# Optimization experiments

Hardware: AMD Instinct MI355X
Metric: run time of the kernel (lower is better)

Reference implementation:

```python
import jax, jax.numpy as jnp
import numpy as np

N, D, P, R, T, K = 200000, 128, 4096, 4, 3, 16

def setup_inputs() -> dict:
    key = jax.random.key(0)
    ks = jax.random.split(key, 9)
    return {
        "node_embeds": jax.random.normal(ks[0], (N, D), jnp.float32),
        "node_pairs": jax.random.randint(ks[1], (P, 2), 0, N),
        "node_type_ids": jax.random.randint(ks[2], (N,), 0, T),
        "neighbor_idx": jax.random.randint(ks[3], (P, 2, R, K), 0, N),
        "delta_t": jax.random.uniform(ks[4], (P, 2, R, K), jnp.float32),
        "W_phi": jax.random.normal(ks[5], (T, D, D), jnp.float32) * 0.05,
        "W_zeta": jax.random.normal(ks[6], (2 * D,), jnp.float32) * 0.05,
        "W_beta_w": jax.random.normal(ks[7], (R, D, D), jnp.float32) * 0.05,
        "W_beta_b": jax.random.normal(ks[8], (R, D), jnp.float32) * 0.05,
    }

def reference(node_embeds, node_pairs, node_type_ids, neighbor_idx, delta_t,
              W_phi, W_zeta, W_beta_w, W_beta_b):
    n = node_embeds.shape[0]
    # per-node type-specific linear: compute all types then select (T small)
    H_all = jnp.einsum('nd,tde->tne', node_embeds, W_phi)        # [T,N,D]
    H = H_all[node_type_ids, jnp.arange(n)]                      # [N,D]
    # micro attention: e = W_zeta([h_n; h_s]) * exp(-dt), softmax over K neighbors
    zn, zs = W_zeta[:D], W_zeta[D:]
    h_n = H[neighbor_idx]                                        # [P,2,R,K,D]
    e_n = jnp.einsum('psrkd,d->psrk', h_n, zn)
    e_s = jnp.einsum('psd,d->ps', H[node_pairs], zs)             # [P,2]
    e = (e_n + e_s[:, :, None, None]) * jnp.exp(-delta_t)        # [P,2,R,K]
    alpha = jax.nn.softmax(e, axis=-1)
    # meso: attention-weighted aggregation per relation, then per-relation linear
    h_nei = node_embeds[neighbor_idx]                            # [P,2,R,K,D]
    h_agg = jnp.einsum('psrk,psrkd->psrd', alpha, h_nei)         # [P,2,R,D]
    h_beta = jnp.einsum('psrd,rde->psre', h_agg, W_beta_w) + W_beta_b
    # macro: average over both pair sides and relations, sigmoid combine
    x_tilde = h_beta.mean(axis=(1, 2))                           # [P,D]
    return jax.nn.sigmoid(x_tilde)
```

## Files before the change

kernel.cpp:

```cpp
#include <hip/hip_runtime.h>
#include <hip/hip_bf16.h>

#define NN 200000
#define D 128
#define P 4096
#define R 4
#define T 3
#define K 16

__device__ __forceinline__ float bf2f(unsigned int u) {
    union { unsigned int i; float f; } c;
    c.i = u << 16;
    return c.f;
}
__device__ __forceinline__ unsigned short f2bf(float x) {
    union { float f; unsigned int i; } c; c.f = x;
    unsigned int r = c.i + 0x7FFFu + ((c.i >> 16) & 1u);
    return (unsigned short)(r >> 16);
}
__device__ __forceinline__ float ldE(const void* p, size_t i, int f32) {
    return f32 ? ((const float*)p)[i] : bf2f(((const unsigned short*)p)[i]);
}
__device__ __forceinline__ void ld8(const void* p, size_t off, int f32, float* o) {
    if (f32) {
        const float* q = (const float*)p + off;
        float4 a = *(const float4*)q;
        float4 b = *(const float4*)(q + 4);
        o[0]=a.x; o[1]=a.y; o[2]=a.z; o[3]=a.w;
        o[4]=b.x; o[5]=b.y; o[6]=b.z; o[7]=b.w;
    } else {
        uint4 r = *(const uint4*)((const unsigned short*)p + off);
        o[0]=bf2f(r.x & 0xffffu); o[1]=bf2f(r.x >> 16);
        o[2]=bf2f(r.y & 0xffffu); o[3]=bf2f(r.y >> 16);
        o[4]=bf2f(r.z & 0xffffu); o[5]=bf2f(r.z >> 16);
        o[6]=bf2f(r.w & 0xffffu); o[7]=bf2f(r.w >> 16);
    }
}

__global__ void prep_kernel(const unsigned short* __restrict__ emb_u,
                            const void* __restrict__ W_phi,
                            const void* __restrict__ W_zeta,
                            int* __restrict__ gflag,
                            float* __restrict__ ws_v, float* __restrict__ ws_u) {
    __shared__ int sbad[2];
    const int tid = threadIdx.x;
    const int t   = blockIdx.x;
    int bad = 0;
    #pragma unroll
    for (int i = 0; i < 4; ++i) {
        unsigned short u = emb_u[(size_t)(blockIdx.x * 512 + tid * 4 + i) * 2 * 97];
        unsigned int e = (u >> 7) & 0xFFu;
        if (e >= 147u) bad = 1;
    }
    int anyb = __any(bad) ? 1 : 0;
    if ((tid & 63) == 0) sbad[tid >> 6] = anyb;
    __syncthreads();
    const int f32 = sbad[0] | sbad[1];
    if (t == 0 && tid == 0) *gflag = f32;

    const int d = tid;
    const size_t rb = (size_t)(t * D + d) * D;
    float av = 0.f, au = 0.f;
    for (int e = 0; e < D; e += 8) {
        float w[8], zn[8], zs[8];
        ld8(W_phi, rb + e, f32, w);
        ld8(W_zeta, e, f32, zn);
        ld8(W_zeta, D + e, f32, zs);
        #pragma unroll
        for (int q = 0; q < 8; ++q) { av += w[q] * zn[q]; au += w[q] * zs[q]; }
    }
    ws_v[t * D + d] = av;
    ws_u[t * D + d] = au;
}

__global__ __launch_bounds__(512, 4) void fused_all(
    const void* __restrict__ emb,
    const int* __restrict__ pairs,
    const int* __restrict__ types,
    const int* __restrict__ nbr,
    const void* __restrict__ dlt,
    const void* __restrict__ W_bw,
    const void* __restrict__ W_bb,
    const float* __restrict__ ws_v,
    const float* __restrict__ ws_u,
    const int* __restrict__ flag,
    void* __restrict__ out)
{
    __shared__ __align__(16) float vsh[T * D];
    __shared__ __align__(16) float ush[T * D];
    __shared__ __align__(16) float gsh[2][R][D];
    __shared__ __align__(16) float gsum[R][D];
    __shared__ __align__(16) float ysh[R][D];

    const int f32  = *flag;
    const int tid  = threadIdx.x;
    const int wv   = tid >> 6;
    const int l    = tid & 63;
    const int s    = wv >> 2;
    const int r    = wv & 3;
    const int p    = blockIdx.x;
    const int rsub = l >> 4;
    const int ch   = l & 15;
    const int base = p * 2 * R * K + s * R * K + r * K;

    const int k   = l & 15;
    const int nb  = nbr[base + k];
    const float dtv = ldE(dlt, (size_t)(base + k), f32);
    const int ns  = pairs[p * 2 + s];

    int snb[4];
    #pragma unroll
    for (int i = 0; i < 4; ++i) snb[i] = __shfl(nb, i * 4 + rsub, 64);

    const unsigned short* eu = (const unsigned short*)emb;
    uint4 cur[4];
    if (!f32) {
        #pragma unroll
        for (int i = 0; i < 4; ++i)
            cur[i] = *(const uint4*)(eu + (size_t)snb[i] * D + ch * 8);
    }
    const int tp = types[nb];
    const int ts = types[ns];

    float ee0, ee1;
    if (!f32) {
        unsigned int w2 = *(const unsigned int*)(eu + (size_t)ns * D + 2 * l);
        ee0 = bf2f(w2 & 0xffffu); ee1 = bf2f(w2 >> 16);
    } else {
        float2 f2 = *(const float2*)((const float*)emb + (size_t)ns * D + 2 * l);
        ee0 = f2.x; ee1 = f2.y;
    }

    for (int i = tid; i < T * D; i += 512) { vsh[i] = ws_v[i]; ush[i] = ws_u[i]; }
    __syncthreads();

    float es;
    {
        float a = ee0 * ush[ts * D + 2 * l] + ee1 * ush[ts * D + 2 * l + 1];
        #pragma unroll
        for (int off = 1; off <= 32; off <<= 1) a += __shfl_xor(a, off, 64);
        es = a;
    }

    float sdt[4]; int stp[4];
    #pragma unroll
    for (int i = 0; i < 4; ++i) {
        sdt[i] = __shfl(dtv, i * 4 + rsub, 64);
        stp[i] = __shfl(tp,  i * 4 + rsub, 64);
    }

    float ef[4];
    if (!f32) {
        #pragma unroll
        for (int i = 0; i < 4; ++i) {
            const float* vp = vsh + stp[i] * D + ch * 8;
            float4 v0 = *(const float4*)vp;
            float4 v1 = *(const float4*)(vp + 4);
            float a = 0.f;
            a += bf2f(cur[i].x & 0xffffu) * v0.x + bf2f(cur[i].x >> 16) * v0.y;
            a += bf2f(cur[i].y & 0xffffu) * v0.z + bf2f(cur[i].y >> 16) * v0.w;
            a += bf2f(cur[i].z & 0xffffu) * v1.x + bf2f(cur[i].z >> 16) * v1.y;
            a += bf2f(cur[i].w & 0xffffu) * v1.z + bf2f(cur[i].w >> 16) * v1.w;
            #pragma unroll
            for (int off = 1; off <= 8; off <<= 1) a += __shfl_xor(a, off, 64);
            ef[i] = (a + es) * __expf(-sdt[i]);
        }
    } else {
        #pragma unroll
        for (int i = 0; i < 4; ++i) {
            const float* vp = vsh + stp[i] * D + ch * 8;
            float rv[8];
            ld8(emb, (size_t)snb[i] * D + ch * 8, 1, rv);
            float a = 0.f;
            #pragma unroll
            for (int q = 0; q < 8; ++q) a += rv[q] * vp[q];
            #pragma unroll
            for (int off = 1; off <= 8; off <<= 1) a += __shfl_xor(a, off, 64);
            ef[i] = (a + es) * __expf(-sdt[i]);
        }
    }

    float m = fmaxf(fmaxf(ef[0], ef[1]), fmaxf(ef[2], ef[3]));
    m = fmaxf(m, __shfl_xor(m, 16, 64));
    m = fmaxf(m, __shfl_xor(m, 32, 64));
    float al[4], ssum = 0.f;
    #pragma unroll
    for (int i = 0; i < 4; ++i) { al[i] = __expf(ef[i] - m); ssum += al[i]; }
    ssum += __shfl_xor(ssum, 16, 64);
    ssum += __shfl_xor(ssum, 32, 64);
    float inv = 1.f / ssum;

    float acc[8] = {0.f,0.f,0.f,0.f,0.f,0.f,0.f,0.f};
    if (!f32) {
        #pragma unroll
        for (int i = 0; i < 4; ++i) {
            float a = al[i] * inv;
            acc[0] += a * bf2f(cur[i].x & 0xffffu); acc[1] += a * bf2f(cur[i].x >> 16);
            acc[2] += a * bf2f(cur[i].y & 0xffffu); acc[3] += a * bf2f(cur[i].y >> 16);
            acc[4] += a * bf2f(cur[i].z & 0xffffu); acc[5] += a * bf2f(cur[i].z >> 16);
            acc[6] += a * bf2f(cur[i].w & 0xffffu); acc[7] += a * bf2f(cur[i].w >> 16);
        }
    } else {
        #pragma unroll
        for (int i = 0; i < 4; ++i) {
            float a = al[i] * inv;
            float rv[8];
            ld8(emb, (size_t)snb[i] * D + ch * 8, 1, rv);
            #pragma unroll
            for (int q = 0; q < 8; ++q) acc[q] += a * rv[q];
        }
    }
    #pragma unroll
    for (int q = 0; q < 8; ++q) {
        acc[q] += __shfl_xor(acc[q], 16, 64);
        acc[q] += __shfl_xor(acc[q], 32, 64);
    }
    if (rsub == 0) {
        *(float4*)(&gsh[s][r][ch * 8])     = make_float4(acc[0], acc[1], acc[2], acc[3]);
        *(float4*)(&gsh[s][r][ch * 8 + 4]) = make_float4(acc[4], acc[5], acc[6], acc[7]);
    }
    __syncthreads();

    {
        const int r2 = tid >> 7, d2 = tid & 127;
        gsum[r2][d2] = gsh[0][r2][d2] + gsh[1][r2][d2];
    }
    __syncthreads();

    float y[8] = {0.f,0.f,0.f,0.f,0.f,0.f,0.f,0.f};
    const int ch8  = l & 7;
    const int dgrp = l >> 3;
    const unsigned short* Wu = (const unsigned short*)W_bw;
    #pragma unroll 4
    for (int dd = 0; dd < 16; ++dd) {
        const int d = dgrp * 16 + ((dd + 2 * dgrp) & 15);
        const float gd = gsum[r][d];
        const size_t wo = ((size_t)(r * D + d)) * D + s * 64 + ch8 * 8;
        if (!f32) {
            uint4 wr = *(const uint4*)(Wu + wo);
            y[0] += gd * bf2f(wr.x & 0xffffu); y[1] += gd * bf2f(wr.x >> 16);
            y[2] += gd * bf2f(wr.y & 0xffffu); y[3] += gd * bf2f(wr.y >> 16);
            y[4] += gd * bf2f(wr.z & 0xffffu); y[5] += gd * bf2f(wr.z >> 16);
            y[6] += gd * bf2f(wr.w & 0xffffu); y[7] += gd * bf2f(wr.w >> 16);
        } else {
            float wb[8]; ld8(W_bw, wo, 1, wb);
            #pragma unroll
            for (int q = 0; q < 8; ++q) y[q] += gd * wb[q];
        }
    }
    #pragma unroll
    for (int q = 0; q < 8; ++q) {
        y[q] += __shfl_xor(y[q], 8, 64);
        y[q] += __shfl_xor(y[q], 16, 64);
        y[q] += __shfl_xor(y[q], 32, 64);
    }
    if (dgrp == 0) {
        *(float4*)(&ysh[r][s * 64 + ch8 * 8])     = make_float4(y[0], y[1], y[2], y[3]);
        *(float4*)(&ysh[r][s * 64 + ch8 * 8 + 4]) = make_float4(y[4], y[5], y[6], y[7]);
    }
    __syncthreads();

    if (wv == 0 && l < 16) {
        const int c = l;
        float bs[8] = {0.f,0.f,0.f,0.f,0.f,0.f,0.f,0.f};
        #pragma unroll
        for (int rr = 0; rr < R; ++rr) {
            float bb[8]; ld8(W_bb, (size_t)rr * D + c * 8, f32, bb);
            #pragma unroll
            for (int q = 0; q < 8; ++q) bs[q] += bb[q];
        }
        float o[8];
        #pragma unroll
        for (int q = 0; q < 8; ++q) {
            const int e = c * 8 + q;
            float x = (ysh[0][e] + ysh[1][e] + ysh[2][e] + ysh[3][e] + 2.f * bs[q]) * 0.125f;
            o[q] = 1.f / (1.f + __expf(-x));
        }
        size_t ob = (size_t)p * D + c * 8;
        if (f32) {
            *(float4*)((float*)out + ob)     = make_float4(o[0], o[1], o[2], o[3]);
            *(float4*)((float*)out + ob + 4) = make_float4(o[4], o[5], o[6], o[7]);
        } else {
            uint4 pk;
            pk.x = (unsigned int)f2bf(o[0]) | ((unsigned int)f2bf(o[1]) << 16);
            pk.y = (unsigned int)f2bf(o[2]) | ((unsigned int)f2bf(o[3]) << 16);
            pk.z = (unsigned int)f2bf(o[4]) | ((unsigned int)f2bf(o[5]) << 16);
            pk.w = (unsigned int)f2bf(o[6]) | ((unsigned int)f2bf(o[7]) << 16);
            *(uint4*)((unsigned short*)out + ob) = pk;
        }
    }
}

extern "C" void kernel_launch(void* const* d_in, const int* in_sizes, int n_in,
                              void* d_out, int out_size, void* d_ws, size_t ws_size,
                              hipStream_t stream) {
    const void* emb    = d_in[0];
    const int*  pairs  = (const int*)d_in[1];
    const int*  types  = (const int*)d_in[2];
    const int*  nbr    = (const int*)d_in[3];
    const void* dlt    = d_in[4];
    const void* W_phi  = d_in[5];
    const void* W_zeta = d_in[6];
    const void* W_bw   = d_in[7];
    const void* W_bb   = d_in[8];

    int*   flag = (int*)d_ws;
    float* ws_v = (float*)d_ws + 64;
    float* ws_u = ws_v + T * D;

    prep_kernel<<<dim3(T), dim3(128), 0, stream>>>((const unsigned short*)emb,
                                                   W_phi, W_zeta, flag, ws_v, ws_u);
    fused_all<<<dim3(P), dim3(512), 0, stream>>>(emb, pairs, types, nbr, dlt,
                                                 W_bw, W_bb, ws_v, ws_u, flag, d_out);
}
```

Before: 268.3 us.

## Process four pairs per block with software-prefetched gathers for the next pair

Each block now handles four pairs in a loop instead of one, with the neighbor index, delta, type and embedding gathers for the next pair issued before the W_beta matvec of the current pair so their latency overlaps. The per-block setup (loading v/u vectors and the summed bias, now staged in shared memory) is amortized over four pairs, and barriers use a custom LDS-only wait. The cost is more registers (launch bounds lowered to 3 blocks per CU), a quarter as many blocks, and a custom barrier that skips waiting on outstanding global loads.

```diff
diff --git a/kernel.cpp b/kernel.cpp
--- a/kernel.cpp
+++ b/kernel.cpp
@@ -7,6 +7,7 @@
 #define R 4
 #define T 3
 #define K 16
+#define NPB 4
 
 __device__ __forceinline__ float bf2f(unsigned int u) {
     union { unsigned int i; float f; } c;
@@ -35,6 +36,12 @@
         o[4]=bf2f(r.z & 0xffffu); o[5]=bf2f(r.z >> 16);
         o[6]=bf2f(r.w & 0xffffu); o[7]=bf2f(r.w >> 16);
     }
+}
+
+__device__ __forceinline__ void lbar() {
+    asm volatile("s_waitcnt lgkmcnt(0)" ::: "memory");
+    __builtin_amdgcn_s_barrier();
+    asm volatile("" ::: "memory");
 }
 
 __global__ void prep_kernel(const unsigned short* __restrict__ emb_u,
@@ -73,7 +80,7 @@
     ws_u[t * D + d] = au;
 }
 
-__global__ __launch_bounds__(512, 4) void fused_all(
+__global__ __launch_bounds__(512, 3) void fused_all(
     const void* __restrict__ emb,
     const int* __restrict__ pairs,
     const int* __restrict__ types,
@@ -91,6 +98,7 @@
     __shared__ __align__(16) float gsh[2][R][D];
     __shared__ __align__(16) float gsum[R][D];
     __shared__ __align__(16) float ysh[R][D];
+    __shared__ __align__(16) float bsh[D];
 
     const int f32  = *flag;
     const int tid  = threadIdx.x;
@@ -98,195 +106,238 @@
     const int l    = tid & 63;
     const int s    = wv >> 2;
     const int r    = wv & 3;
-    const int p    = blockIdx.x;
     const int rsub = l >> 4;
     const int ch   = l & 15;
-    const int base = p * 2 * R * K + s * R * K + r * K;
-
-    const int k   = l & 15;
-    const int nb  = nbr[base + k];
-    const float dtv = ldE(dlt, (size_t)(base + k), f32);
-    const int ns  = pairs[p * 2 + s];
-
-    int snb[4];
-    #pragma unroll
-    for (int i = 0; i < 4; ++i) snb[i] = __shfl(nb, i * 4 + rsub, 64);
-
+    const int k    = l & 15;
+    const int p0   = blockIdx.x * NPB;
     const unsigned short* eu = (const unsigned short*)emb;
-    uint4 cur[4];
-    if (!f32) {
-        #pragma unroll
-        for (int i = 0; i < 4; ++i)
-            cur[i] = *(const uint4*)(eu + (size_t)snb[i] * D + ch * 8);
-    }
-    const int tp = types[nb];
-    const int ts = types[ns];
-
-    float ee0, ee1;
-    if (!f32) {
-        unsigned int w2 = *(const unsigned int*)(eu + (size_t)ns * D + 2 * l);
-        ee0 = bf2f(w2 & 0xffffu); ee1 = bf2f(w2 >> 16);
-    } else {
-        float2 f2 = *(const float2*)((const float*)emb + (size_t)ns * D + 2 * l);
-        ee0 = f2.x; ee1 = f2.y;
-    }
-
+
+    int   nb, ns, tp, ts;
+    float dtv, ee0, ee1;
+    uint4 cur[4] = {};
+    {
+        const int base0 = p0 * 2 * R * K + s * R * K + r * K;
+        nb  = nbr[base0 + k];
+        dtv = ldE(dlt, (size_t)(base0 + k), f32);
+        ns  = pairs[p0 * 2 + s];
+        tp  = types[nb];
+        ts  = types[ns];
+        if (!f32) {
+            int snb_[4];
+            #pragma unroll
+            for (int i = 0; i < 4; ++i) snb_[i] = __shfl(nb, i * 4 + rsub, 64);
+            #pragma unroll
+            for (int i = 0; i < 4; ++i)
+                cur[i] = *(const uint4*)(eu + (size_t)snb_[i] * D + ch * 8);
+            unsigned int w2 = *(const unsigned int*)(eu + (size_t)ns * D + 2 * l);
+            ee0 = bf2f(w2 & 0xffffu); ee1 = bf2f(w2 >> 16);
+        } else {
+            float2 f2 = *(const float2*)((const float*)emb + (size_t)ns * D + 2 * l);
+            ee0 = f2.x; ee1 = f2.y;
+        }
+    }
     for (int i = tid; i < T * D; i += 512) { vsh[i] = ws_v[i]; ush[i] = ws_u[i]; }
+    if (tid < D) {
+        float b = 0.f;
+        #pragma unroll
+        for (int rr = 0; rr < R; ++rr) b += ldE(W_bb, (size_t)rr * D + tid, f32);
+        bsh[tid] = b;
+    }
     __syncthreads();
 
-    float es;
-    {
-        float a = ee0 * ush[ts * D + 2 * l] + ee1 * ush[ts * D + 2 * l + 1];
-        #pragma unroll
-        for (int off = 1; off <= 32; off <<= 1) a += __shfl_xor(a, off, 64);
-        es = a;
-    }
-
-    float sdt[4]; int stp[4];
-    #pragma unroll
-    for (int i = 0; i < 4; ++i) {
-        sdt[i] = __shfl(dtv, i * 4 + rsub, 64);
-        stp[i] = __shfl(tp,  i * 4 + rsub, 64);
-    }
-
-    float ef[4];
-    if (!f32) {
+    for (int t = 0; t < NPB; ++t) {
+        const int p = p0 + t;
+
+        int nb2 = 0, ns2 = 0; float dtv2 = 0.f;
+        if (t < NPB - 1) {
+            const int base2 = (p + 1) * 2 * R * K + s * R * K + r * K;
+            nb2  = nbr[base2 + k];
+            dtv2 = ldE(dlt, (size_t)(base2 + k), f32);
+            ns2  = pairs[(p + 1) * 2 + s];
+        }
+
+        float es;
+        {
+            float a = ee0 * ush[ts * D + 2 * l] + ee1 * ush[ts * D + 2 * l + 1];
+            #pragma unroll
+            for (int off = 1; off <= 32; off <<= 1) a += __shfl_xor(a, off, 64);
+            es = a;
+        }
+
+        float sdt[4]; int stp[4];
         #pragma unroll
         for (int i = 0; i < 4; ++i) {
-            const float* vp = vsh + stp[i] * D + ch * 8;
-            float4 v0 = *(const float4*)vp;
-            float4 v1 = *(const float4*)(vp + 4);
-            float a = 0.f;
-            a += bf2f(cur[i].x & 0xffffu) * v0.x + bf2f(cur[i].x >> 16) * v0.y;
-            a += bf2f(cur[i].y & 0xffffu) * v0.z + bf2f(cur[i].y >> 16) * v0.w;
-            a += bf2f(cur[i].z & 0xffffu) * v1.x + bf2f(cur[i].z >> 16) * v1.y;
-            a += bf2f(cur[i].w & 0xffffu) * v1.z + bf2f(cur[i].w >> 16) * v1.w;
-            #pragma unroll
-            for (int off = 1; off <= 8; off <<= 1) a += __shfl_xor(a, off, 64);
-            ef[i] = (a + es) * __expf(-sdt[i]);
-        }
-    } else {
-        #pragma unroll
-        for (int i = 0; i < 4; ++i) {
-            const float* vp = vsh + stp[i] * D + ch * 8;
-            float rv[8];
-            ld8(emb, (size_t)snb[i] * D + ch * 8, 1, rv);
-            float a = 0.f;
-            #pragma unroll
-            for (int q = 0; q < 8; ++q) a += rv[q] * vp[q];
-            #pragma unroll
-            for (int off = 1; off <= 8; off <<= 1) a += __shfl_xor(a, off, 64);
-            ef[i] = (a + es) * __expf(-sdt[i]);
-        }
-    }
-
-    float m = fmaxf(fmaxf(ef[0], ef[1]), fmaxf(ef[2], ef[3]));
-    m = fmaxf(m, __shfl_xor(m, 16, 64));
-    m = fmaxf(m, __shfl_xor(m, 32, 64));
-    float al[4], ssum = 0.f;
-    #pragma unroll
-    for (int i = 0; i < 4; ++i) { al[i] = __expf(ef[i] - m); ssum += al[i]; }
-    ssum += __shfl_xor(ssum, 16, 64);
-    ssum += __shfl_xor(ssum, 32, 64);
-    float inv = 1.f / ssum;
-
-    float acc[8] = {0.f,0.f,0.f,0.f,0.f,0.f,0.f,0.f};
-    if (!f32) {
-        #pragma unroll
-        for (int i = 0; i < 4; ++i) {
-            float a = al[i] * inv;
-            acc[0] += a * bf2f(cur[i].x & 0xffffu); acc[1] += a * bf2f(cur[i].x >> 16);
-            acc[2] += a * bf2f(cur[i].y & 0xffffu); acc[3] += a * bf2f(cur[i].y >> 16);
-            acc[4] += a * bf2f(cur[i].z & 0xffffu); acc[5] += a * bf2f(cur[i].z >> 16);
-            acc[6] += a * bf2f(cur[i].w & 0xffffu); acc[7] += a * bf2f(cur[i].w >> 16);
-        }
-    } else {
-        #pragma unroll
-        for (int i = 0; i < 4; ++i) {
-            float a = al[i] * inv;
-            float rv[8];
-            ld8(emb, (size_t)snb[i] * D + ch * 8, 1, rv);
-            #pragma unroll
-            for (int q = 0; q < 8; ++q) acc[q] += a * rv[q];
-        }
-    }
-    #pragma unroll
-    for (int q = 0; q < 8; ++q) {
-        acc[q] += __shfl_xor(acc[q], 16, 64);
-        acc[q] += __shfl_xor(acc[q], 32, 64);
-    }
-    if (rsub == 0) {
-        *(float4*)(&gsh[s][r][ch * 8])     = make_float4(acc[0], acc[1], acc[2], acc[3]);
-        *(float4*)(&gsh[s][r][ch * 8 + 4]) = make_float4(acc[4], acc[5], acc[6], acc[7]);
-    }
-    __syncthreads();
-
-    {
-        const int r2 = tid >> 7, d2 = tid & 127;
-        gsum[r2][d2] = gsh[0][r2][d2] + gsh[1][r2][d2];
-    }
-    __syncthreads();
-
-    float y[8] = {0.f,0.f,0.f,0.f,0.f,0.f,0.f,0.f};
-    const int ch8  = l & 7;
-    const int dgrp = l >> 3;
-    const unsigned short* Wu = (const unsigned short*)W_bw;
-    #pragma unroll 4
-    for (int dd = 0; dd < 16; ++dd) {
-        const int d = dgrp * 16 + ((dd + 2 * dgrp) & 15);
-        const float gd = gsum[r][d];
-        const size_t wo = ((size_t)(r * D + d)) * D + s * 64 + ch8 * 8;
+            sdt[i] = __shfl(dtv, i * 4 + rsub, 64);
+            stp[i] = __shfl(tp,  i * 4 + rsub, 64);
+        }
+
+        float ef[4];
         if (!f32) {
-            uint4 wr = *(const uint4*)(Wu + wo);
-            y[0] += gd * bf2f(wr.x & 0xffffu); y[1] += gd * bf2f(wr.x >> 16);
-            y[2] += gd * bf2f(wr.y & 0xffffu); y[3] += gd * bf2f(wr.y >> 16);
-            y[4] += gd * bf2f(wr.z & 0xffffu); y[5] += gd * bf2f(wr.z >> 16);
-            y[6] += gd * bf2f(wr.w & 0xffffu); y[7] += gd * bf2f(wr.w >> 16);
+            #pragma unroll
+            for (int i = 0; i < 4; ++i) {
+                const float* vp = vsh + stp[i] * D + ch * 8;
+                float4 v0 = *(const float4*)vp;
+                float4 v1 = *(const float4*)(vp + 4);
+                float a = 0.f;
+                a += bf2f(cur[i].x & 0xffffu) * v0.x + bf2f(cur[i].x >> 16) * v0.y;
+                a += bf2f(cur[i].y & 0xffffu) * v0.z + bf2f(cur[i].y >> 16) * v0.w;
+                a += bf2f(cur[i].z & 0xffffu) * v1.x + bf2f(cur[i].z >> 16) * v1.y;
+                a += bf2f(cur[i].w & 0xffffu) * v1.z + bf2f(cur[i].w >> 16) * v1.w;
+                #pragma unroll
+                for (int off = 1; off <= 8; off <<= 1) a += __shfl_xor(a, off, 64);
+                ef[i] = (a + es) * __expf(-sdt[i]);
+            }
         } else {
-            float wb[8]; ld8(W_bw, wo, 1, wb);
-            #pragma unroll
-            for (int q = 0; q < 8; ++q) y[q] += gd * wb[q];
-        }
-    }
-    #pragma unroll
-    for (int q = 0; q < 8; ++q) {
-        y[q] += __shfl_xor(y[q], 8, 64);
-        y[q] += __shfl_xor(y[q], 16, 64);
-        y[q] += __shfl_xor(y[q], 32, 64);
-    }
-    if (dgrp == 0) {
-        *(float4*)(&ysh[r][s * 64 + ch8 * 8])     = make_float4(y[0], y[1], y[2], y[3]);
-        *(float4*)(&ysh[r][s * 64 + ch8 * 8 + 4]) = make_float4(y[4], y[5], y[6], y[7]);
-    }
-    __syncthreads();
-
-    if (wv == 0 && l < 16) {
-        const int c = l;
-        float bs[8] = {0.f,0.f,0.f,0.f,0.f,0.f,0.f,0.f};
-        #pragma unroll
-        for (int rr = 0; rr < R; ++rr) {
-            float bb[8]; ld8(W_bb, (size_t)rr * D + c * 8, f32, bb);
-            #pragma unroll
-            for (int q = 0; q < 8; ++q) bs[q] += bb[q];
-        }
-        float o[8];
+            int snbL[4];
+            #pragma unroll
+            for (int i = 0; i < 4; ++i) snbL[i] = __shfl(nb, i * 4 + rsub, 64);
+            #pragma unroll
+            for (int i = 0; i < 4; ++i) {
+                const float* vp = vsh + stp[i] * D + ch * 8;
+                float rv[8];
+                ld8(emb, (size_t)snbL[i] * D + ch * 8, 1, rv);
+                float a = 0.f;
+                #pragma unroll
+                for (int q = 0; q < 8; ++q) a += rv[q] * vp[q];
+                #pragma unroll
+                for (int off = 1; off <= 8; off <<= 1) a += __shfl_xor(a, off, 64);
+                ef[i] = (a + es) * __expf(-sdt[i]);
+            }
+        }
+
+        float m = fmaxf(fmaxf(ef[0], ef[1]), fmaxf(ef[2], ef[3]));
+        m = fmaxf(m, __shfl_xor(m, 16, 64));
+        m = fmaxf(m, __shfl_xor(m, 32, 64));
+        float al[4], ssum = 0.f;
+        #pragma unroll
+        for (int i = 0; i < 4; ++i) { al[i] = __expf(ef[i] - m); ssum += al[i]; }
+        ssum += __shfl_xor(ssum, 16, 64);
+        ssum += __shfl_xor(ssum, 32, 64);
+        float inv = 1.f / ssum;
+
+        float acc[8] = {0.f,0.f,0.f,0.f,0.f,0.f,0.f,0.f};
+        if (!f32) {
+            #pragma unroll
+            for (int i = 0; i < 4; ++i) {
+                float a = al[i] * inv;
+                acc[0] += a * bf2f(cur[i].x & 0xffffu); acc[1] += a * bf2f(cur[i].x >> 16);
+                acc[2] += a * bf2f(cur[i].y & 0xffffu); acc[3] += a * bf2f(cur[i].y >> 16);
+                acc[4] += a * bf2f(cur[i].z & 0xffffu); acc[5] += a * bf2f(cur[i].z >> 16);
+                acc[6] += a * bf2f(cur[i].w & 0xffffu); acc[7] += a * bf2f(cur[i].w >> 16);
+            }
+        } else {
+            int snbL[4];
+            #pragma unroll
+            for (int i = 0; i < 4; ++i) snbL[i] = __shfl(nb, i * 4 + rsub, 64);
+            #pragma unroll
+            for (int i = 0; i < 4; ++i) {
+                float a = al[i] * inv;
+                float rv[8];
+                ld8(emb, (size_t)snbL[i] * D + ch * 8, 1, rv);
+                #pragma unroll
+                for (int q = 0; q < 8; ++q) acc[q] += a * rv[q];
+            }
+        }
         #pragma unroll
         for (int q = 0; q < 8; ++q) {
-            const int e = c * 8 + q;
-            float x = (ysh[0][e] + ysh[1][e] + ysh[2][e] + ysh[3][e] + 2.f * bs[q]) * 0.125f;
-            o[q] = 1.f / (1.f + __expf(-x));
-        }
-        size_t ob = (size_t)p * D + c * 8;
-        if (f32) {
-            *(float4*)((float*)out + ob)     = make_float4(o[0], o[1], o[2], o[3]);
-            *(float4*)((float*)out + ob + 4) = make_float4(o[4], o[5], o[6], o[7]);
-        } else {
-            uint4 pk;
-            pk.x = (unsigned int)f2bf(o[0]) | ((unsigned int)f2bf(o[1]) << 16);
-            pk.y = (unsigned int)f2bf(o[2]) | ((unsigned int)f2bf(o[3]) << 16);
-            pk.z = (unsigned int)f2bf(o[4]) | ((unsigned int)f2bf(o[5]) << 16);
-            pk.w = (unsigned int)f2bf(o[6]) | ((unsigned int)f2bf(o[7]) << 16);
-            *(uint4*)((unsigned short*)out + ob) = pk;
+            acc[q] += __shfl_xor(acc[q], 16, 64);
+            acc[q] += __shfl_xor(acc[q], 32, 64);
+        }
+        if (rsub == 0) {
+            *(float4*)(&gsh[s][r][ch * 8])     = make_float4(acc[0], acc[1], acc[2], acc[3]);
+            *(float4*)(&gsh[s][r][ch * 8 + 4]) = make_float4(acc[4], acc[5], acc[6], acc[7]);
+        }
+        lbar();
+
+        {
+            const int r2 = tid >> 7, d2 = tid & 127;
+            gsum[r2][d2] = gsh[0][r2][d2] + gsh[1][r2][d2];
+        }
+        lbar();
+
+        int tp2 = 0, ts2 = 0; float ee20 = 0.f, ee21 = 0.f;
+        uint4 cur2[4] = {};
+        if (t < NPB - 1) {
+            tp2 = types[nb2];
+            ts2 = types[ns2];
+            if (!f32) {
+                int snb2[4];
+                #pragma unroll
+                for (int i = 0; i < 4; ++i) snb2[i] = __shfl(nb2, i * 4 + rsub, 64);
+                #pragma unroll
+                for (int i = 0; i < 4; ++i)
+                    cur2[i] = *(const uint4*)(eu + (size_t)snb2[i] * D + ch * 8);
+                unsigned int w2 = *(const unsigned int*)(eu + (size_t)ns2 * D + 2 * l);
+                ee20 = bf2f(w2 & 0xffffu); ee21 = bf2f(w2 >> 16);
+            } else {
+                float2 f2 = *(const float2*)((const float*)emb + (size_t)ns2 * D + 2 * l);
+                ee20 = f2.x; ee21 = f2.y;
+            }
+        }
+
+        float y[8] = {0.f,0.f,0.f,0.f,0.f,0.f,0.f,0.f};
+        const int ch8  = l & 7;
+        const int dgrp = l >> 3;
+        const unsigned short* Wu = (const unsigned short*)W_bw;
+        #pragma unroll 4
+        for (int dd = 0; dd < 16; ++dd) {
+            const int d = dgrp * 16 + ((dd + 2 * dgrp) & 15);
+            const float gd = gsum[r][d];
+            const size_t wo = ((size_t)(r * D + d)) * D + s * 64 + ch8 * 8;
+            if (!f32) {
+                uint4 wr = *(const uint4*)(Wu + wo);
+                y[0] += gd * bf2f(wr.x & 0xffffu); y[1] += gd * bf2f(wr.x >> 16);
+                y[2] += gd * bf2f(wr.y & 0xffffu); y[3] += gd * bf2f(wr.y >> 16);
+                y[4] += gd * bf2f(wr.z & 0xffffu); y[5] += gd * bf2f(wr.z >> 16);
+                y[6] += gd * bf2f(wr.w & 0xffffu); y[7] += gd * bf2f(wr.w >> 16);
+            } else {
+                float wb[8]; ld8(W_bw, wo, 1, wb);
+                #pragma unroll
+                for (int q = 0; q < 8; ++q) y[q] += gd * wb[q];
+            }
+        }
+        #pragma unroll
+        for (int q = 0; q < 8; ++q) {
+            y[q] += __shfl_xor(y[q], 8, 64);
+            y[q] += __shfl_xor(y[q], 16, 64);
+            y[q] += __shfl_xor(y[q], 32, 64);
+        }
+        if (dgrp == 0) {
+            *(float4*)(&ysh[r][s * 64 + ch8 * 8])     = make_float4(y[0], y[1], y[2], y[3]);
+            *(float4*)(&ysh[r][s * 64 + ch8 * 8 + 4]) = make_float4(y[4], y[5], y[6], y[7]);
+        }
+        lbar();
+
+        if (wv == 0 && l < 16) {
+            const int c = l;
+            float o[8];
+            #pragma unroll
+            for (int q = 0; q < 8; ++q) {
+                const int e = c * 8 + q;
+                float x = (ysh[0][e] + ysh[1][e] + ysh[2][e] + ysh[3][e]
+                           + 2.f * bsh[e]) * 0.125f;
+                o[q] = 1.f / (1.f + __expf(-x));
+            }
+            size_t ob = (size_t)p * D + c * 8;
+            if (f32) {
+                *(float4*)((float*)out + ob)     = make_float4(o[0], o[1], o[2], o[3]);
+                *(float4*)((float*)out + ob + 4) = make_float4(o[4], o[5], o[6], o[7]);
+            } else {
+                uint4 pk;
+                pk.x = (unsigned int)f2bf(o[0]) | ((unsigned int)f2bf(o[1]) << 16);
+                pk.y = (unsigned int)f2bf(o[2]) | ((unsigned int)f2bf(o[3]) << 16);
+                pk.z = (unsigned int)f2bf(o[4]) | ((unsigned int)f2bf(o[5]) << 16);
+                pk.w = (unsigned int)f2bf(o[6]) | ((unsigned int)f2bf(o[7]) << 16);
+                *(uint4*)((unsigned short*)out + ob) = pk;
+            }
+        }
+        lbar();
+
+        if (t < NPB - 1) {
+            nb = nb2; dtv = dtv2; ns = ns2; tp = tp2; ts = ts2;
+            ee0 = ee20; ee1 = ee21;
+            #pragma unroll
+            for (int i = 0; i < 4; ++i) cur[i] = cur2[i];
         }
     }
 }
@@ -310,6 +361,6 @@
 
     prep_kernel<<<dim3(T), dim3(128), 0, stream>>>((const unsigned short*)emb,
                                                    W_phi, W_zeta, flag, ws_v, ws_u);
-    fused_all<<<dim3(P), dim3(512), 0, stream>>>(emb, pairs, types, nbr, dlt,
-                                                 W_bw, W_bb, ws_v, ws_u, flag, d_out);
-}
+    fused_all<<<dim3(P / NPB), dim3(512), 0, stream>>>(emb, pairs, types, nbr, dlt,
+                                                       W_bw, W_bb, ws_v, ws_u, flag, d_out);
+}
```

New measurement: 302.9 us. 1.13x slower.
